# Kernel tuning notes

Hardware: AMD Instinct MI355X
Metric: run time of the kernel (lower is better)

The kernel has to match this reference:

```python
import jax, jax.numpy as jnp
import numpy as np

B, C, N, K, G = 2, 128, 8192, 16, 8
D = C // G
EPS = 1e-5


def _bn(t, g, b, m, v, axis=1):
    # eval-mode BatchNorm: (t - mean) / sqrt(var + eps) * gamma + beta, per channel
    shp = [1] * t.ndim
    shp[axis] = -1
    return (t - m.reshape(shp)) * jax.lax.rsqrt(v.reshape(shp) + EPS) * g.reshape(shp) + b.reshape(shp)


def _knn(xyz, k):
    # brute-force KNN (torch fallback path): xyz (B,3,N) -> idx (B,N,k), includes self
    pts = jnp.transpose(xyz, (0, 2, 1))  # (B,N,3)
    sq = jnp.sum(pts * pts, axis=-1)  # (B,N)
    d2 = sq[:, :, None] + sq[:, None, :] - 2.0 * jnp.einsum('bnc,bmc->bnm', pts, pts)
    _, idx = jax.lax.top_k(-d2, k)  # k smallest squared distances
    return idx


def setup_inputs() -> dict:
    ks = jax.random.split(jax.random.key(0), 16)
    rn = lambda i, s, sc=1.0: jax.random.normal(ks[i], s, jnp.float32) * sc
    sC = C ** -0.5
    return {
        'x': rn(0, (B, C, N)),
        'xyz': rn(1, (B, 3, N)),
        'wq': rn(2, (C, C), sC),
        'bnq_g': jnp.ones((C,)), 'bnq_b': jnp.zeros((C,)), 'bnq_m': jnp.zeros((C,)), 'bnq_v': jnp.ones((C,)),
        'wk': rn(3, (C, C), sC),
        'bnk_g': jnp.ones((C,)), 'bnk_b': jnp.zeros((C,)), 'bnk_m': jnp.zeros((C,)), 'bnk_v': jnp.ones((C,)),
        'wv': rn(4, (C, C), sC),
        'pe_w1': rn(5, (C, 3), 3 ** -0.5),
        'pe_bn_g': jnp.ones((C,)), 'pe_bn_b': jnp.zeros((C,)), 'pe_bn_m': jnp.zeros((C,)), 'pe_bn_v': jnp.ones((C,)),
        'pe_w2': rn(6, (C, C), sC),
        'we_w1': rn(7, (G, C), sC),
        'we_bn_g': jnp.ones((G,)), 'we_bn_b': jnp.zeros((G,)), 'we_bn_m': jnp.zeros((G,)), 'we_bn_v': jnp.ones((G,)),
        'we_w2': rn(8, (G, G), G ** -0.5),
        'wo': rn(9, (C, C), sC),
        'bno_g': jnp.ones((C,)), 'bno_b': jnp.zeros((C,)), 'bno_m': jnp.zeros((C,)), 'bno_v': jnp.ones((C,)),
    }


def reference(x, xyz, wq, bnq_g, bnq_b, bnq_m, bnq_v, wk, bnk_g, bnk_b, bnk_m, bnk_v, wv,
              pe_w1, pe_bn_g, pe_bn_b, pe_bn_m, pe_bn_v, pe_w2,
              we_w1, we_bn_g, we_bn_b, we_bn_m, we_bn_v, we_w2,
              wo, bno_g, bno_b, bno_m, bno_v):
    # q/k/v projections: 1x1 Conv1d == channel matmul
    q = jax.nn.relu(_bn(jnp.einsum('oc,bcn->bon', wq, x), bnq_g, bnq_b, bnq_m, bnq_v))  # (B,C,N)
    kf = jax.nn.relu(_bn(jnp.einsum('oc,bcn->bon', wk, x), bnk_g, bnk_b, bnk_m, bnk_v))
    vf = jnp.einsum('oc,bcn->bon', wv, x)

    idx = _knn(xyz, K)  # (B,N,K)
    bi = jnp.arange(B)[:, None, None]
    kn = jnp.transpose(kf[bi, :, idx], (0, 3, 1, 2))   # (B,C,N,K)
    vn = jnp.transpose(vf[bi, :, idx], (0, 3, 1, 2))   # (B,C,N,K)
    xn = jnp.transpose(xyz[bi, :, idx], (0, 3, 1, 2))  # (B,3,N,K)

    rel = kn - q[:, :, :, None]
    rel_pos = xn - xyz[:, :, :, None]

    # positional encoding MLP (1x1 Conv2d chain)
    pe = jnp.einsum('oc,bcnk->bonk', pe_w2,
                    jax.nn.relu(_bn(jnp.einsum('oc,bcnk->bonk', pe_w1, rel_pos),
                                    pe_bn_g, pe_bn_b, pe_bn_m, pe_bn_v)))
    rel = rel + pe
    vn = vn + pe

    # grouped attention weights over K neighbors
    w = jnp.einsum('hg,bgnk->bhnk', we_w2,
                   jax.nn.relu(_bn(jnp.einsum('gc,bcnk->bgnk', we_w1, rel),
                                   we_bn_g, we_bn_b, we_bn_m, we_bn_v)))  # (B,G,N,K)
    w = jax.nn.softmax(w, axis=-1)

    vg = vn.reshape(B, G, D, N, K)
    out = jnp.einsum('bgdnk,bgnk->bgdn', vg, w).reshape(B, C, N)
    return _bn(jnp.einsum('oc,bcn->bon', wo, out), bno_g, bno_b, bno_m, bno_v)
```

## Files before the change

kernel.cpp:

```cpp
#include <hip/hip_runtime.h>
#include <math.h>

typedef unsigned int u32;
typedef unsigned long long u64;

#define BATCH 2
#define CH 128
#define NPTS 8192
#define KNB 16
#define GRP 8
#define EPSN 1e-5f

#define WS_A     0
#define WS_PW1   4096
#define WS_WE2   6144
#define WS_PTS   8192
#define WS_EQ    270336
#define WS_EK    794624
#define WS_IDX   1318912
#define WS_VFT   2367488

__device__ __forceinline__ float d2f(float4 a, float4 b){
  #pragma clang fp contract(off)
  float dot = a.x*b.x + a.y*b.y + a.z*b.z;
  return (a.w + b.w) - 2.0f*dot;
}
__device__ __forceinline__ u64 shfl_xor_u64(u64 v, int m){
  int lo = __shfl_xor((int)(u32)v, m);
  int hi = __shfl_xor((int)(u32)(v >> 32), m);
  return (((u64)(u32)hi) << 32) | (u32)lo;
}
__device__ __forceinline__ int mbcnt64(u64 bm){
  return (int)__builtin_amdgcn_mbcnt_hi((u32)(bm >> 32),
          __builtin_amdgcn_mbcnt_lo((u32)(bm & 0xFFFFFFFFull), 0u));
}
__device__ __forceinline__ u32 mono32(float d2){
  u32 db = __float_as_uint(d2);
  return (db & 0x80000000u) ? ~db : (db | 0x80000000u);
}

__global__ __launch_bounds__(256) void k0_precomp(
    const float* we_w1, const float* pe_w2, const float* pe_w1,
    const float* we_g, const float* we_v,
    const float* pe_g, const float* pe_b, const float* pe_m, const float* pe_v,
    const float* we_w2, float* wsA, float4* wsPW1, float* wsWE2){
  int t = threadIdx.x;
  for (int i = t; i < 1024; i += 256){
    int g = i >> 7, h = i & 127;
    float s = 0.f;
    for (int c = 0; c < 128; ++c) s = fmaf(we_w1[g*128+c], pe_w2[c*128+h], s);
    float sg = we_g[g] / sqrtf(we_v[g] + EPSN);
    wsA[i] = s * sg;
  }
  if (t < 128){
    float s = pe_g[t] / sqrtf(pe_v[t] + EPSN);
    float bb = pe_b[t] - pe_m[t] * s;
    wsPW1[t] = make_float4(s*pe_w1[t*3+0], s*pe_w1[t*3+1], s*pe_w1[t*3+2], bb);
  }
  if (t < 64) wsWE2[t] = we_w2[t];
}

__global__ __launch_bounds__(256) void k1_pts(const float* xyz, float4* pts){
  int id = blockIdx.x*256 + threadIdx.x;
  if (id >= BATCH*NPTS) return;
  int b = id >> 13, n = id & (NPTS-1);
  float x = xyz[(b*3+0)*NPTS + n];
  float y = xyz[(b*3+1)*NPTS + n];
  float z = xyz[(b*3+2)*NPTS + n];
  float sq;
  {
    #pragma clang fp contract(off)
    sq = (x*x + y*y) + z*z;
  }
  pts[id] = make_float4(x, y, z, sq);
}

#define K2PTS 32
__global__ __launch_bounds__(256) void k2_proj(
    const float* x, const float* wq, const float* wk, const float* wv,
    const float* bnq_g, const float* bnq_b, const float* bnq_m, const float* bnq_v,
    const float* bnk_g, const float* bnk_b, const float* bnk_m, const float* bnk_v,
    const float* we_w1,
    const float* we_g, const float* we_b, const float* we_m, const float* we_v,
    float* eqT, float* ekT, float* vfT){
  __shared__ __align__(16) float qk2[K2PTS][129];
  __shared__ float bnS[128], bnB[128];
  int t = threadIdx.x;
  int mat = blockIdx.x % 3;
  int tmp = blockIdx.x / 3;
  int b   = tmp / (NPTS/K2PTS);
  int n0  = (tmp % (NPTS/K2PTS)) * K2PTS;
  int p = t & 31, og = t >> 5;
  const float* xp = x + (size_t)b*CH*NPTS + n0 + p;
  const float* W = (mat == 0) ? wq : ((mat == 1) ? wk : wv);
  if (mat < 2 && t < 128){
    const float* g_ = mat==0 ? bnq_g : bnk_g;
    const float* b_ = mat==0 ? bnq_b : bnk_b;
    const float* m_ = mat==0 ? bnq_m : bnk_m;
    const float* v_ = mat==0 ? bnq_v : bnk_v;
    float s = g_[t] / sqrtf(v_[t] + EPSN);
    bnS[t] = s;
    bnB[t] = b_[t] - m_[t] * s;
  }
  __syncthreads();
  float acc[16];
  #pragma unroll
  for (int ii = 0; ii < 16; ++ii) acc[ii] = 0.f;
  for (int dd = 0; dd < 32; ++dd){
    float x0 = xp[(size_t)(4*dd+0)*NPTS];
    float x1 = xp[(size_t)(4*dd+1)*NPTS];
    float x2 = xp[(size_t)(4*dd+2)*NPTS];
    float x3 = xp[(size_t)(4*dd+3)*NPTS];
    #pragma unroll
    for (int ii = 0; ii < 16; ++ii){
      int o = og*16 + ii;
      float4 wu = *(const float4*)&W[o*128 + 4*dd];
      acc[ii] = fmaf(wu.x, x0, acc[ii]);
      acc[ii] = fmaf(wu.y, x1, acc[ii]);
      acc[ii] = fmaf(wu.z, x2, acc[ii]);
      acc[ii] = fmaf(wu.w, x3, acc[ii]);
    }
  }
  #pragma unroll
  for (int ii = 0; ii < 16; ++ii){
    int o = og*16 + ii;
    float v = acc[ii];
    if (mat < 2) v = fmaxf(fmaf(bnS[o], v, bnB[o]), 0.f);
    qk2[p][o] = v;
  }
  __syncthreads();
  if (mat < 2){
    int g = t >> 5, pp = t & 31;
    float sg = we_g[g] / sqrtf(we_v[g] + EPSN);
    float tg = we_b[g] - we_m[g] * sg;
    float s = 0.f;
    for (int c4 = 0; c4 < 32; ++c4){
      float4 wv4 = *(const float4*)&we_w1[g*128 + 4*c4];
      float4 qv4 = *(const float4*)&qk2[pp][4*c4];
      s = fmaf(wv4.x, qv4.x, s);
      s = fmaf(wv4.y, qv4.y, s);
      s = fmaf(wv4.z, qv4.z, s);
      s = fmaf(wv4.w, qv4.w, s);
    }
    float val = (mat == 0) ? (tg - sg*s) : (sg*s);
    float* dst = (mat == 0) ? eqT : ekT;
    dst[(b*NPTS + n0 + pp)*8 + g] = val;
  } else {
    #pragma unroll
    for (int i = 0; i < 4; ++i){
      int f = t + 256*i;
      int pp = f >> 5, c4 = (f & 31)*4;
      float4 v = *(const float4*)&qk2[pp][c4];
      *(float4*)&vfT[((size_t)b*NPTS + n0 + pp)*CH + c4] = v;
    }
  }
}

#define QW   2
#define QPB  8
#define CAPQ 288
__global__ __launch_bounds__(256) void k3_knn(const float4* pts, int* idxout){
  __shared__ u64 smBuf[4][QW][CAPQ];
  int t = threadIdx.x;
  int wv = t >> 6, lane = t & 63;
  int b  = blockIdx.x / (NPTS/QPB);
  int q0 = (blockIdx.x % (NPTS/QPB)) * QPB + wv*QW;
  const float4* P = pts + b*NPTS;

  #pragma unroll
  for (int s = 0; s < QW*CAPQ/64; ++s){
    int f = s*64 + lane;
    smBuf[wv][f / CAPQ][f % CAPQ] = ~0ull;
  }

  float4 qp[QW];
  #pragma unroll
  for (int i = 0; i < QW; ++i) qp[i] = P[q0 + i];

  float T[QW];
  {
    float v0 = 3.402823466e38f, v1 = 3.402823466e38f;
    #pragma unroll
    for (int j = 0; j < 16; ++j){
      float4 c = P[lane + 64*j];
      v0 = fminf(v0, d2f(qp[0], c));
      v1 = fminf(v1, d2f(qp[1], c));
    }
    float t0 = v0, t1 = v1;
    #pragma unroll
    for (int r = 0; r < 16; ++r){
      float m0 = v0, m1 = v1;
      #pragma unroll
      for (int msk = 1; msk <= 32; msk <<= 1){
        m0 = fminf(m0, __shfl_xor(m0, msk));
        m1 = fminf(m1, __shfl_xor(m1, msk));
      }
      if (v0 == m0) v0 = 3.402823466e38f;
      if (v1 == m1) v1 = 3.402823466e38f;
      t0 = m0; t1 = m1;
    }
    T[0] = t0; T[1] = t1;
  }

  float Tlo[QW], Thi[QW]; int cnt[QW];
  #pragma unroll
  for (int i = 0; i < QW; ++i){ Tlo[i] = -3.0e38f; Thi[i] = 3.0e38f; cnt[i] = 0; }
  auto step = [&](float4 c, u32 m, int i){
    float d2 = d2f(qp[i], c);
    bool pred = d2 <= T[i];
    u64 bm = __ballot(pred);
    if (bm){
      int cc = __popcll(bm);
      if (pred && cnt[i] + cc <= CAPQ){
        int pos = cnt[i] + mbcnt64(bm);
        smBuf[wv][i][pos] = (((u64)mono32(d2)) << 32) | m;
      }
      cnt[i] += cc;
    }
  };
  bool anybad = true;
  for (int att = 0; att < 16 && anybad; ++att){
    #pragma unroll
    for (int i = 0; i < QW; ++i) cnt[i] = 0;
    float4 c0 = P[lane], c1 = P[64 + lane], c2 = P[128 + lane], c3 = P[192 + lane];
    for (int base = 0; base < NPTS; base += 256){
      float4 e0 = c0, e1 = c1, e2 = c2, e3 = c3;
      int nb = base + 256;
      if (nb < NPTS){
        c0 = P[nb       + lane];
        c1 = P[nb +  64 + lane];
        c2 = P[nb + 128 + lane];
        c3 = P[nb + 192 + lane];
      }
      #pragma unroll
      for (int i = 0; i < QW; ++i){
        step(e0, (u32)(base       + lane), i);
        step(e1, (u32)(base +  64 + lane), i);
        step(e2, (u32)(base + 128 + lane), i);
        step(e3, (u32)(base + 192 + lane), i);
      }
    }
    anybad = false;
    #pragma unroll
    for (int i = 0; i < QW; ++i){
      if (cnt[i] > CAPQ){
        Thi[i] = T[i];
        T[i] = (Tlo[i] > -3.0e38f) ? 0.5f*(Tlo[i] + Thi[i])
                                   : ((T[i] > 0.f) ? T[i]*0.5f : T[i]*2.0f - 1.0f);
        anybad = true;
      } else if (cnt[i] < 16){
        Tlo[i] = T[i];
        T[i] = 0.5f*(Tlo[i] + Thi[i]);
        anybad = true;
      }
    }
  }

  {
    int cq0 = cnt[0] < CAPQ ? cnt[0] : CAPQ;
    int cq1 = cnt[1] < CAPQ ? cnt[1] : CAPQ;
    u64 a0, a1, a2, a3, a4, b0, b1, b2, b3, b4;
    a0 = (lane       < cq0) ? smBuf[wv][0][lane      ] : ~0ull;
    a1 = (lane +  64 < cq0) ? smBuf[wv][0][lane +  64] : ~0ull;
    a2 = (lane + 128 < cq0) ? smBuf[wv][0][lane + 128] : ~0ull;
    a3 = (lane + 192 < cq0) ? smBuf[wv][0][lane + 192] : ~0ull;
    a4 = (lane + 256 < cq0) ? smBuf[wv][0][lane + 256] : ~0ull;
    b0 = (lane       < cq1) ? smBuf[wv][1][lane      ] : ~0ull;
    b1 = (lane +  64 < cq1) ? smBuf[wv][1][lane +  64] : ~0ull;
    b2 = (lane + 128 < cq1) ? smBuf[wv][1][lane + 128] : ~0ull;
    b3 = (lane + 192 < cq1) ? smBuf[wv][1][lane + 192] : ~0ull;
    b4 = (lane + 256 < cq1) ? smBuf[wv][1][lane + 256] : ~0ull;
    #define CE_(x,y) { if (y < x){ u64 tm_ = x; x = y; y = tm_; } }
    CE_(a0,a1) CE_(a1,a2) CE_(a2,a3) CE_(a3,a4)
    CE_(a0,a1) CE_(a1,a2) CE_(a2,a3)
    CE_(a0,a1) CE_(a1,a2)
    CE_(a0,a1)
    CE_(b0,b1) CE_(b1,b2) CE_(b2,b3) CE_(b3,b4)
    CE_(b0,b1) CE_(b1,b2) CE_(b2,b3)
    CE_(b0,b1) CE_(b1,b2)
    CE_(b0,b1)
    #undef CE_
    int nq0 = q0, nq1 = q0 + 1;
    #pragma unroll
    for (int r = 0; r < 16; ++r){
      u64 g0 = a0, g1 = b0;
      #pragma unroll
      for (int msk = 1; msk <= 32; msk <<= 1){
        u64 o0 = shfl_xor_u64(g0, msk);
        u64 o1 = shfl_xor_u64(g1, msk);
        g0 = (o0 < g0) ? o0 : g0;
        g1 = (o1 < g1) ? o1 : g1;
      }
      if (a0 == g0){ a0 = a1; a1 = a2; a2 = a3; a3 = a4; a4 = ~0ull; }
      if (b0 == g1){ b0 = b1; b1 = b2; b2 = b3; b3 = b4; b4 = ~0ull; }
      if (lane == 0){
        idxout[(b*NPTS + nq0)*16 + r] = (g0 == ~0ull) ? nq0 : (int)(g0 & (u32)(NPTS-1));
        idxout[(b*NPTS + nq1)*16 + r] = (g1 == ~0ull) ? nq1 : (int)(g1 & (u32)(NPTS-1));
      }
    }
  }
}

#define H2S 136
__global__ __launch_bounds__(256, 4) void k4_attn(
    const float4* pts, const float* eqT, const float* ekT, const int* idxw,
    const float* vfT, const float* wsA, const float4* wsPW1, const float* wsWE2,
    const float* pe_w2, const float* wo,
    const float* bno_g, const float* bno_b, const float* bno_m, const float* bno_v,
    float* out){
  __shared__ __align__(16) float4 smW1[128];
  __shared__ __align__(16) float4 smP[4][16];
  __shared__ int   smJ[4][16];
  __shared__ float smw[4][16][8];
  __shared__ __align__(16) float smH[4][8][H2S];
  __shared__ __align__(16) float smOutv[4][128];
  int t = threadIdx.x;
  int wv = t >> 6, lane = t & 63;
  int b  = blockIdx.x >> 11;
  int n0 = (blockIdx.x & 2047) * 4;
  if (t < 128) smW1[t] = wsPW1[t];
  __syncthreads();

  int n = n0 + wv;
  int gq = b*NPTS + n;
  int k = lane >> 2, q = lane & 3;

  {
    float4 pn  = pts[gq];
    float4 eqa = *(const float4*)&eqT[gq*8];
    float4 eqb = *(const float4*)&eqT[gq*8+4];
    int j = idxw[gq*16 + k] & (NPTS-1);
    int gj = b*NPTS + j;
    float4 pj  = pts[gj];
    float4 eka = *(const float4*)&ekT[gj*8];
    float4 ekb = *(const float4*)&ekT[gj*8+4];
    float rx = pj.x - pn.x, ry = pj.y - pn.y, rz = pj.z - pn.z;
    if (q == 0){
      smP[wv][k] = make_float4(rx, ry, rz, 0.f);
      smJ[wv][k] = j;
    }
    float ee[8] = {eka.x+eqa.x, eka.y+eqa.y, eka.z+eqa.z, eka.w+eqa.w,
                   ekb.x+eqb.x, ekb.y+eqb.y, ekb.z+eqb.z, ekb.w+eqb.w};
    float lp[8] = {0.f,0.f,0.f,0.f,0.f,0.f,0.f,0.f};
    #pragma unroll
    for (int i = 0; i < 8; ++i){
      int hb = 4*q + 16*i;
      float4 w1;
      w1 = smW1[hb+0]; float hv0 = fmaxf(fmaf(w1.x, rx, fmaf(w1.y, ry, fmaf(w1.z, rz, w1.w))), 0.f);
      w1 = smW1[hb+1]; float hv1 = fmaxf(fmaf(w1.x, rx, fmaf(w1.y, ry, fmaf(w1.z, rz, w1.w))), 0.f);
      w1 = smW1[hb+2]; float hv2 = fmaxf(fmaf(w1.x, rx, fmaf(w1.y, ry, fmaf(w1.z, rz, w1.w))), 0.f);
      w1 = smW1[hb+3]; float hv3 = fmaxf(fmaf(w1.x, rx, fmaf(w1.y, ry, fmaf(w1.z, rz, w1.w))), 0.f);
      #pragma unroll
      for (int g = 0; g < 8; ++g){
        float4 a4 = *(const float4*)&wsA[g*128 + hb];
        lp[g] = fmaf(a4.x, hv0, lp[g]);
        lp[g] = fmaf(a4.y, hv1, lp[g]);
        lp[g] = fmaf(a4.z, hv2, lp[g]);
        lp[g] = fmaf(a4.w, hv3, lp[g]);
      }
    }
    #pragma unroll
    for (int g = 0; g < 8; ++g){
      lp[g] += __shfl_xor(lp[g], 1);
      lp[g] += __shfl_xor(lp[g], 2);
      lp[g] = fmaxf(lp[g] + ee[g], 0.f);
    }
    float lo0 = 0.f, lo1 = 0.f;
    #pragma unroll
    for (int g = 0; g < 8; ++g){
      lo0 = fmaf(wsWE2[(2*q+0)*8 + g], lp[g], lo0);
      lo1 = fmaf(wsWE2[(2*q+1)*8 + g], lp[g], lo1);
    }
    float m0 = lo0, m1 = lo1;
    #pragma unroll
    for (int msk = 4; msk <= 32; msk <<= 1){
      m0 = fmaxf(m0, __shfl_xor(m0, msk));
      m1 = fmaxf(m1, __shfl_xor(m1, msk));
    }
    float e0 = __expf(lo0 - m0), e1 = __expf(lo1 - m1);
    float s0 = e0, s1 = e1;
    #pragma unroll
    for (int msk = 4; msk <= 32; msk <<= 1){
      s0 += __shfl_xor(s0, msk);
      s1 += __shfl_xor(s1, msk);
    }
    smw[wv][k][2*q+0] = e0 / s0;
    smw[wv][k][2*q+1] = e1 / s1;
  }

  {
    int g3 = lane >> 3, hh = lane & 7;
    float4 H4[4];
    #pragma unroll
    for (int ii = 0; ii < 4; ++ii) H4[ii] = make_float4(0.f,0.f,0.f,0.f);
    for (int kk = 0; kk < 16; ++kk){
      float4 r4 = smP[wv][kk];
      float wg  = smw[wv][kk][g3];
      #pragma unroll
      for (int ii = 0; ii < 4; ++ii){
        int hb = 4*hh + 32*ii;
        float4 w1;
        w1 = smW1[hb+0]; float hv0 = fmaxf(fmaf(w1.x, r4.x, fmaf(w1.y, r4.y, fmaf(w1.z, r4.z, w1.w))), 0.f);
        w1 = smW1[hb+1]; float hv1 = fmaxf(fmaf(w1.x, r4.x, fmaf(w1.y, r4.y, fmaf(w1.z, r4.z, w1.w))), 0.f);
        w1 = smW1[hb+2]; float hv2 = fmaxf(fmaf(w1.x, r4.x, fmaf(w1.y, r4.y, fmaf(w1.z, r4.z, w1.w))), 0.f);
        w1 = smW1[hb+3]; float hv3 = fmaxf(fmaf(w1.x, r4.x, fmaf(w1.y, r4.y, fmaf(w1.z, r4.z, w1.w))), 0.f);
        H4[ii].x = fmaf(wg, hv0, H4[ii].x);
        H4[ii].y = fmaf(wg, hv1, H4[ii].y);
        H4[ii].z = fmaf(wg, hv2, H4[ii].z);
        H4[ii].w = fmaf(wg, hv3, H4[ii].w);
      }
    }
    #pragma unroll
    for (int ii = 0; ii < 4; ++ii)
      *(float4*)&smH[wv][g3][4*hh + 32*ii] = H4[ii];
  }
  __syncthreads();

  if (t < 128){
    int c = t, g = c >> 4;
    float acc[4] = {0.f, 0.f, 0.f, 0.f};
    for (int i = 0; i < 32; ++i){
      float4 pw = *(const float4*)&pe_w2[c*128 + 4*i];
      #pragma unroll
      for (int pt = 0; pt < 4; ++pt){
        float4 h4 = *(const float4*)&smH[pt][g][4*i];
        acc[pt] = fmaf(pw.x, h4.x, acc[pt]);
        acc[pt] = fmaf(pw.y, h4.y, acc[pt]);
        acc[pt] = fmaf(pw.z, h4.z, acc[pt]);
        acc[pt] = fmaf(pw.w, h4.w, acc[pt]);
      }
    }
    #pragma unroll
    for (int pt = 0; pt < 4; ++pt){
      #pragma unroll
      for (int kk = 0; kk < 16; ++kk){
        int jj = smJ[pt][kk];
        float wgk = smw[pt][kk][g];
        acc[pt] = fmaf(wgk, vfT[((size_t)b*NPTS + jj)*CH + c], acc[pt]);
      }
      smOutv[pt][c] = acc[pt];
    }
  }
  __syncthreads();

  if (t < 128){
    int o = t;
    float so = bno_g[o] / sqrtf(bno_v[o] + EPSN);
    float bo = bno_b[o] - bno_m[o] * so;
    float fa[4] = {0.f, 0.f, 0.f, 0.f};
    for (int i = 0; i < 32; ++i){
      float4 pw = *(const float4*)&wo[o*128 + 4*i];
      #pragma unroll
      for (int pt = 0; pt < 4; ++pt){
        float4 h4 = *(const float4*)&smOutv[pt][4*i];
        fa[pt] = fmaf(pw.x, h4.x, fa[pt]);
        fa[pt] = fmaf(pw.y, h4.y, fa[pt]);
        fa[pt] = fmaf(pw.z, h4.z, fa[pt]);
        fa[pt] = fmaf(pw.w, h4.w, fa[pt]);
      }
    }
    float4 st;
    st.x = fmaf(so, fa[0], bo);
    st.y = fmaf(so, fa[1], bo);
    st.z = fmaf(so, fa[2], bo);
    st.w = fmaf(so, fa[3], bo);
    *(float4*)&out[((size_t)b*CH + o)*NPTS + n0] = st;
  }
}

extern "C" void kernel_launch(void* const* d_in, const int* in_sizes, int n_in,
                              void* d_out, int out_size, void* d_ws, size_t ws_size,
                              hipStream_t stream){
  const float* x     = (const float*)d_in[0];
  const float* xyz   = (const float*)d_in[1];
  const float* wq    = (const float*)d_in[2];
  const float* bnq_g = (const float*)d_in[3];
  const float* bnq_b = (const float*)d_in[4];
  const float* bnq_m = (const float*)d_in[5];
  const float* bnq_v = (const float*)d_in[6];
  const float* wk    = (const float*)d_in[7];
  const float* bnk_g = (const float*)d_in[8];
  const float* bnk_b = (const float*)d_in[9];
  const float* bnk_m = (const float*)d_in[10];
  const float* bnk_v = (const float*)d_in[11];
  const float* wv    = (const float*)d_in[12];
  const float* pe_w1 = (const float*)d_in[13];
  const float* pe_g  = (const float*)d_in[14];
  const float* pe_b  = (const float*)d_in[15];
  const float* pe_m  = (const float*)d_in[16];
  const float* pe_v  = (const float*)d_in[17];
  const float* pe_w2 = (const float*)d_in[18];
  const float* we_w1 = (const float*)d_in[19];
  const float* we_g  = (const float*)d_in[20];
  const float* we_b  = (const float*)d_in[21];
  const float* we_m  = (const float*)d_in[22];
  const float* we_v  = (const float*)d_in[23];
  const float* we_w2 = (const float*)d_in[24];
  const float* wo    = (const float*)d_in[25];
  const float* bno_g = (const float*)d_in[26];
  const float* bno_b = (const float*)d_in[27];
  const float* bno_m = (const float*)d_in[28];
  const float* bno_v = (const float*)d_in[29];

  char* ws = (char*)d_ws;
  float*  wsA   = (float*)(ws + WS_A);
  float4* wsPW1 = (float4*)(ws + WS_PW1);
  float*  wsWE2 = (float*)(ws + WS_WE2);
  float4* pts   = (float4*)(ws + WS_PTS);
  float*  eqT   = (float*)(ws + WS_EQ);
  float*  ekT   = (float*)(ws + WS_EK);
  int*    idxw  = (int*)(ws + WS_IDX);
  float*  vfT   = (float*)(ws + WS_VFT);
  float*  outp  = (float*)d_out;

  k0_precomp<<<dim3(1), dim3(256), 0, stream>>>(we_w1, pe_w2, pe_w1, we_g, we_v,
                                                pe_g, pe_b, pe_m, pe_v, we_w2,
                                                wsA, wsPW1, wsWE2);
  k1_pts<<<dim3(64), dim3(256), 0, stream>>>(xyz, pts);
  k2_proj<<<dim3(BATCH*(NPTS/K2PTS)*3), dim3(256), 0, stream>>>(x, wq, wk, wv,
                                               bnq_g, bnq_b, bnq_m, bnq_v,
                                               bnk_g, bnk_b, bnk_m, bnk_v,
                                               we_w1, we_g, we_b, we_m, we_v,
                                               eqT, ekT, vfT);
  k3_knn<<<dim3(BATCH*(NPTS/QPB)), dim3(256), 0, stream>>>(pts, idxw);
  k4_attn<<<dim3(BATCH*(NPTS/4)), dim3(256), 0, stream>>>(pts, eqT, ekT, idxw, vfT,
                                                wsA, wsPW1, wsWE2, pe_w2, wo,
                                                bno_g, bno_b, bno_m, bno_v, outp);
}
```

Before: 354.6 us.

## Use per-lane candidate slots in KNN filter instead of ballot-compacted buffer

The KNN candidate collection now lets each lane keep up to five candidates in its own shared-memory slots instead of compacting survivors wave-wide with ballot and mbcnt. This removes a ballot, popcount and prefix count per distance test. The threshold search is changed too: it starts at half of the 16th-smallest sample minimum, counts candidates with a shuffle reduction, and treats any single lane overflowing its slots as a signal to lower the threshold. The per-lane cap can trigger more threshold retries when candidates cluster in one lane, and those retries each rescan all points.

```diff
diff --git a/kernel.cpp b/kernel.cpp
--- a/kernel.cpp
+++ b/kernel.cpp
@@ -29,10 +29,6 @@
   int lo = __shfl_xor((int)(u32)v, m);
   int hi = __shfl_xor((int)(u32)(v >> 32), m);
   return (((u64)(u32)hi) << 32) | (u32)lo;
-}
-__device__ __forceinline__ int mbcnt64(u64 bm){
-  return (int)__builtin_amdgcn_mbcnt_hi((u32)(bm >> 32),
-          __builtin_amdgcn_mbcnt_lo((u32)(bm & 0xFFFFFFFFull), 0u));
 }
 __device__ __forceinline__ u32 mono32(float d2){
   u32 db = __float_as_uint(d2);
@@ -158,9 +154,9 @@
 
 #define QW   2
 #define QPB  8
-#define CAPQ 288
+#define SLOT 5
 __global__ __launch_bounds__(256) void k3_knn(const float4* pts, int* idxout){
-  __shared__ u64 smBuf[4][QW][CAPQ];
+  __shared__ u64 smBuf[4][QW][64][SLOT];
   int t = threadIdx.x;
   int wv = t >> 6, lane = t & 63;
   int b  = blockIdx.x / (NPTS/QPB);
@@ -168,23 +164,20 @@
   const float4* P = pts + b*NPTS;
 
   #pragma unroll
-  for (int s = 0; s < QW*CAPQ/64; ++s){
-    int f = s*64 + lane;
-    smBuf[wv][f / CAPQ][f % CAPQ] = ~0ull;
-  }
-
-  float4 qp[QW];
-  #pragma unroll
-  for (int i = 0; i < QW; ++i) qp[i] = P[q0 + i];
-
-  float T[QW];
+  for (int i = 0; i < QW; ++i)
+    #pragma unroll
+    for (int s = 0; s < SLOT; ++s) smBuf[wv][i][lane][s] = ~0ull;
+
+  float4 qp0 = P[q0], qp1 = P[q0 + 1];
+
+  float Tg0, Tg1;
   {
     float v0 = 3.402823466e38f, v1 = 3.402823466e38f;
     #pragma unroll
     for (int j = 0; j < 16; ++j){
       float4 c = P[lane + 64*j];
-      v0 = fminf(v0, d2f(qp[0], c));
-      v1 = fminf(v1, d2f(qp[1], c));
+      v0 = fminf(v0, d2f(qp0, c));
+      v1 = fminf(v1, d2f(qp1, c));
     }
     float t0 = v0, t1 = v1;
     #pragma unroll
@@ -199,77 +192,85 @@
       if (v1 == m1) v1 = 3.402823466e38f;
       t0 = m0; t1 = m1;
     }
-    T[0] = t0; T[1] = t1;
-  }
-
-  float Tlo[QW], Thi[QW]; int cnt[QW];
-  #pragma unroll
-  for (int i = 0; i < QW; ++i){ Tlo[i] = -3.0e38f; Thi[i] = 3.0e38f; cnt[i] = 0; }
-  auto step = [&](float4 c, u32 m, int i){
-    float d2 = d2f(qp[i], c);
-    bool pred = d2 <= T[i];
-    u64 bm = __ballot(pred);
-    if (bm){
-      int cc = __popcll(bm);
-      if (pred && cnt[i] + cc <= CAPQ){
-        int pos = cnt[i] + mbcnt64(bm);
-        smBuf[wv][i][pos] = (((u64)mono32(d2)) << 32) | m;
-      }
-      cnt[i] += cc;
-    }
-  };
+    Tg0 = t0; Tg1 = t1;
+  }
+  float T0 = 0.5f*Tg0, T1 = 0.5f*Tg1;
+  float Tlo0 = -3.0e38f, Thi0 = 3.0e38f, Tlo1 = -3.0e38f, Thi1 = 3.0e38f;
+  int c0 = 0, c1 = 0;
+
   bool anybad = true;
   for (int att = 0; att < 16 && anybad; ++att){
-    #pragma unroll
-    for (int i = 0; i < QW; ++i) cnt[i] = 0;
-    float4 c0 = P[lane], c1 = P[64 + lane], c2 = P[128 + lane], c3 = P[192 + lane];
+    c0 = 0; c1 = 0;
+    float4 ch0 = P[lane], ch1 = P[64 + lane], ch2 = P[128 + lane], ch3 = P[192 + lane];
     for (int base = 0; base < NPTS; base += 256){
-      float4 e0 = c0, e1 = c1, e2 = c2, e3 = c3;
+      float4 e0 = ch0, e1 = ch1, e2 = ch2, e3 = ch3;
       int nb = base + 256;
       if (nb < NPTS){
-        c0 = P[nb       + lane];
-        c1 = P[nb +  64 + lane];
-        c2 = P[nb + 128 + lane];
-        c3 = P[nb + 192 + lane];
-      }
-      #pragma unroll
-      for (int i = 0; i < QW; ++i){
-        step(e0, (u32)(base       + lane), i);
-        step(e1, (u32)(base +  64 + lane), i);
-        step(e2, (u32)(base + 128 + lane), i);
-        step(e3, (u32)(base + 192 + lane), i);
-      }
-    }
+        ch0 = P[nb       + lane];
+        ch1 = P[nb +  64 + lane];
+        ch2 = P[nb + 128 + lane];
+        ch3 = P[nb + 192 + lane];
+      }
+      auto stp = [&](float4 e, u32 m){
+        float d0 = d2f(qp0, e);
+        if (d0 <= T0){
+          if (c0 < SLOT) smBuf[wv][0][lane][c0] = (((u64)mono32(d0)) << 32) | m;
+          ++c0;
+        }
+        float d1 = d2f(qp1, e);
+        if (d1 <= T1){
+          if (c1 < SLOT) smBuf[wv][1][lane][c1] = (((u64)mono32(d1)) << 32) | m;
+          ++c1;
+        }
+      };
+      stp(e0, (u32)(base       + lane));
+      stp(e1, (u32)(base +  64 + lane));
+      stp(e2, (u32)(base + 128 + lane));
+      stp(e3, (u32)(base + 192 + lane));
+    }
+    u64 of0 = __ballot(c0 > SLOT);
+    u64 of1 = __ballot(c1 > SLOT);
+    int pk = (c0 < SLOT ? c0 : SLOT) | ((c1 < SLOT ? c1 : SLOT) << 16);
+    #pragma unroll
+    for (int msk = 1; msk <= 32; msk <<= 1) pk += __shfl_xor(pk, msk);
+    int tot0 = pk & 0xFFFF, tot1 = pk >> 16;
     anybad = false;
-    #pragma unroll
-    for (int i = 0; i < QW; ++i){
-      if (cnt[i] > CAPQ){
-        Thi[i] = T[i];
-        T[i] = (Tlo[i] > -3.0e38f) ? 0.5f*(Tlo[i] + Thi[i])
-                                   : ((T[i] > 0.f) ? T[i]*0.5f : T[i]*2.0f - 1.0f);
-        anybad = true;
-      } else if (cnt[i] < 16){
-        Tlo[i] = T[i];
-        T[i] = 0.5f*(Tlo[i] + Thi[i]);
-        anybad = true;
-      }
+    if (of0){
+      Thi0 = T0;
+      T0 = (Tlo0 > -3.0e38f) ? 0.5f*(Tlo0 + Thi0)
+                             : ((T0 > 0.f) ? T0*0.5f : T0*2.0f - 1.0f);
+      anybad = true;
+    } else if (tot0 < 16){
+      Tlo0 = T0;
+      T0 = (Thi0 < 3.0e38f) ? 0.5f*(Tlo0 + Thi0) : Tg0;
+      anybad = true;
+    }
+    if (of1){
+      Thi1 = T1;
+      T1 = (Tlo1 > -3.0e38f) ? 0.5f*(Tlo1 + Thi1)
+                             : ((T1 > 0.f) ? T1*0.5f : T1*2.0f - 1.0f);
+      anybad = true;
+    } else if (tot1 < 16){
+      Tlo1 = T1;
+      T1 = (Thi1 < 3.0e38f) ? 0.5f*(Tlo1 + Thi1) : Tg1;
+      anybad = true;
     }
   }
 
   {
-    int cq0 = cnt[0] < CAPQ ? cnt[0] : CAPQ;
-    int cq1 = cnt[1] < CAPQ ? cnt[1] : CAPQ;
+    int cq0 = c0 < SLOT ? c0 : SLOT;
+    int cq1 = c1 < SLOT ? c1 : SLOT;
     u64 a0, a1, a2, a3, a4, b0, b1, b2, b3, b4;
-    a0 = (lane       < cq0) ? smBuf[wv][0][lane      ] : ~0ull;
-    a1 = (lane +  64 < cq0) ? smBuf[wv][0][lane +  64] : ~0ull;
-    a2 = (lane + 128 < cq0) ? smBuf[wv][0][lane + 128] : ~0ull;
-    a3 = (lane + 192 < cq0) ? smBuf[wv][0][lane + 192] : ~0ull;
-    a4 = (lane + 256 < cq0) ? smBuf[wv][0][lane + 256] : ~0ull;
-    b0 = (lane       < cq1) ? smBuf[wv][1][lane      ] : ~0ull;
-    b1 = (lane +  64 < cq1) ? smBuf[wv][1][lane +  64] : ~0ull;
-    b2 = (lane + 128 < cq1) ? smBuf[wv][1][lane + 128] : ~0ull;
-    b3 = (lane + 192 < cq1) ? smBuf[wv][1][lane + 192] : ~0ull;
-    b4 = (lane + 256 < cq1) ? smBuf[wv][1][lane + 256] : ~0ull;
+    a0 = (0 < cq0) ? smBuf[wv][0][lane][0] : ~0ull;
+    a1 = (1 < cq0) ? smBuf[wv][0][lane][1] : ~0ull;
+    a2 = (2 < cq0) ? smBuf[wv][0][lane][2] : ~0ull;
+    a3 = (3 < cq0) ? smBuf[wv][0][lane][3] : ~0ull;
+    a4 = (4 < cq0) ? smBuf[wv][0][lane][4] : ~0ull;
+    b0 = (0 < cq1) ? smBuf[wv][1][lane][0] : ~0ull;
+    b1 = (1 < cq1) ? smBuf[wv][1][lane][1] : ~0ull;
+    b2 = (2 < cq1) ? smBuf[wv][1][lane][2] : ~0ull;
+    b3 = (3 < cq1) ? smBuf[wv][1][lane][3] : ~0ull;
+    b4 = (4 < cq1) ? smBuf[wv][1][lane][4] : ~0ull;
     #define CE_(x,y) { if (y < x){ u64 tm_ = x; x = y; y = tm_; } }
     CE_(a0,a1) CE_(a1,a2) CE_(a2,a3) CE_(a3,a4)
     CE_(a0,a1) CE_(a1,a2) CE_(a2,a3)
```

Result: slower. 375.3 us (+5.8%).
